# Performance work log

Measured on AMD Instinct MI355X. Metric: run time of the kernel, lower is better.

## Reference

```python
import jax, jax.numpy as jnp
import numpy as np
from jax.scipy.special import logsumexp

B, S, H, T, M = 64, 512, 768, 500, 8
POSITION_WEIGHT = 0.6
LABEL_SMOOTH = 0.1
GAMMA = 2.0


def setup_inputs() -> dict:
    key = jax.random.key(0)
    ks = jax.random.split(key, 12)
    hidden = jax.random.normal(ks[0], (B, S, H), jnp.float32)  # BERT sequence_output stand-in
    lengths = jax.random.randint(ks[1], (B,), S // 2, S + 1)
    attention_mask = (jnp.arange(S)[None, :] < lengths[:, None]).astype(jnp.int32)
    position_labels = jax.random.randint(ks[2], (B, S), 0, 3).astype(jnp.int32)
    type_labels = jax.random.randint(ks[3], (B, M), 0, T).astype(jnp.int32)
    starts = jax.random.randint(ks[4], (B, M), 1, S // 2)
    ends = starts + jax.random.randint(ks[5], (B, M), 2, 8)
    valid = jax.random.uniform(ks[6], (B, M)) < 0.8  # some (batch, span) slots unused, like the original sum()>0 filter
    target_positions = jnp.where(valid[..., None], jnp.stack([starts, ends], -1), 0).astype(jnp.int32)
    # CRF params exactly as hardcoded in __init__
    trans = jnp.array([[-5.0, 20.0, -10000.0], [-50.0, 0.0, 50.0], [0.0, -50.0, 30.0]], jnp.float32)
    start_trans = jnp.array([0.0, 0.0, -10000.0], jnp.float32)
    end_trans = jnp.array([0.0, -100.0, 0.0], jnp.float32)
    return {
        'hidden': hidden,
        'attention_mask': attention_mask,
        'position_labels': position_labels,
        'type_labels': type_labels,
        'target_positions': target_positions,
        'bi_label_weight': jnp.asarray(0.5, jnp.float32),
        'W_pos': 0.02 * jax.random.normal(ks[7], (H, 3), jnp.float32),
        'b_pos': jnp.zeros((3,), jnp.float32),
        'start_trans': start_trans,
        'end_trans': end_trans,
        'trans': trans,
        'att_W1': 0.02 * jax.random.normal(ks[8], (H, 64), jnp.float32),
        'att_b1': jnp.zeros((64,), jnp.float32),
        'att_W2': 0.02 * jax.random.normal(ks[9], (64, 1), jnp.float32),
        'att_b2': jnp.zeros((1,), jnp.float32),
        'W_type': 0.02 * jax.random.normal(ks[10], (H, T), jnp.float32),
        'b_type': jnp.zeros((T,), jnp.float32),
    }


def crf_nll(em, labels, mask, start_trans, end_trans, trans):
    # torchcrf-style masked negative log-likelihood, reduction='none'
    maskf = mask.astype(em.dtype)
    emit = jnp.take_along_axis(em, labels[..., None], -1)[..., 0]  # [B,S]
    emit_score = (emit * maskf).sum(1)
    tr = trans[labels[:, :-1], labels[:, 1:]]  # [B,S-1]
    tr_score = (tr * maskf[:, 1:]).sum(1)
    last = mask.sum(1) - 1
    last_tags = jnp.take_along_axis(labels, last[:, None], 1)[:, 0]
    score = start_trans[labels[:, 0]] + emit_score + tr_score + end_trans[last_tags]
    # log partition via scan over time
    alpha = start_trans[None, :] + em[:, 0]  # [B,3]
    def step(alpha, xs):
        em_t, m_t = xs
        nxt = logsumexp(alpha[:, :, None] + trans[None, :, :] + em_t[:, None, :], axis=1)
        return jnp.where(m_t[:, None], nxt, alpha), None
    alpha, _ = jax.lax.scan(step, alpha, (em[:, 1:].transpose(1, 0, 2), mask[:, 1:].T))
    logZ = logsumexp(alpha + end_trans[None, :], axis=-1)
    return logZ - score  # = -log_likelihood


def reference(hidden, attention_mask, position_labels, type_labels, target_positions,
              bi_label_weight, W_pos, b_pos, start_trans, end_trans, trans,
              att_W1, att_b1, att_W2, att_b2, W_type, b_type):
    mask = attention_mask.astype(bool)
    emissions = hidden @ W_pos + b_pos  # [B,S,3]
    w = jnp.where(position_labels > 0, 1.0 + bi_label_weight, 1.0)[..., None]
    em_w = emissions * w
    position_loss = crf_nll(em_w, position_labels, mask, start_trans, end_trans, trans).mean()

    # span attention pooling, batched over all (B,M) pairs instead of the Python loop
    scores = (jnp.tanh(hidden @ att_W1 + att_b1) @ att_W2 + att_b2)[..., 0]  # [B,S]
    starts = target_positions[..., 0]
    ends = target_positions[..., 1]
    valid = target_positions.sum(-1) > 0  # [B,M]
    pos = jnp.arange(hidden.shape[1])
    span_mask = (pos[None, None, :] >= starts[..., None]) & (pos[None, None, :] < ends[..., None])  # [B,M,S]
    att = jnp.where(span_mask, scores[:, None, :], -1e9)
    aw = jax.nn.softmax(att, axis=-1)  # per-span softmax == softmax over the gathered span
    pooled = jnp.einsum('bms,bsh->bmh', aw, hidden)  # [B,M,H]
    logits = pooled @ W_type + b_type  # [B,M,T]

    # label-smoothed focal loss over valid spans only
    nT = logits.shape[-1]
    onehot = jax.nn.one_hot(type_labels, nT, dtype=logits.dtype)
    smooth = onehot * (1.0 - LABEL_SMOOTH) + LABEL_SMOOTH / nT
    logp = jax.nn.log_softmax(logits, axis=-1)
    probs = jnp.exp(logp)
    ce = -(smooth * logp).sum(-1)
    pt = (smooth * probs).sum(-1)
    focal = ce * (1.0 - pt) ** GAMMA
    v = valid.astype(focal.dtype)
    type_loss = (focal * v).sum() / jnp.maximum(v.sum(), 1.0) * 10.0

    joint = POSITION_WEIGHT * position_loss + (1.0 - POSITION_WEIGHT) * type_loss
    return jnp.stack([joint, position_loss, type_loss])
```

## Files before the change

### kernel.cpp

```cpp
#include <hip/hip_runtime.h>

#define L2E 1.44269504088896340736f
#define LN2 0.69314718055994530942f
#define NEGB -1e30f

typedef float f32x4 __attribute__((ext_vector_type(4)));
typedef __bf16 bf16x8 __attribute__((ext_vector_type(8)));

static constexpr int NB = 64, NS = 512, NH = 768, NT = 500, NM = 8;

static constexpr size_t WT_ALL_OFF   = 0;
static constexpr size_t WT_TYPE_OFF  = 122880;
static constexpr size_t EM_T_OFF     = 909312;
static constexpr size_t SCORES_OFF   = 1302528;
static constexpr size_t LABELS_T_OFF = 1433600;
static constexpr size_t LEN_OFF      = 1564672;
static constexpr size_t SCAL_OFF     = 3399936;
static constexpr size_t MATM_OFF     = 3400192;
static constexpr size_t PSC_OFF      = 3547648;

__device__ __forceinline__ unsigned short f2bf(float f) {
  unsigned u = __builtin_bit_cast(unsigned, f);
  u += 0x7FFFu + ((u >> 16) & 1u);
  return (unsigned short)(u >> 16);
}
__device__ __forceinline__ float sel3(float a, float b, float c, int i) {
  return i == 0 ? a : (i == 1 ? b : c);
}
__device__ __forceinline__ float lse3(float x, float y, float z) {
  float m = fmaxf(fmaxf(x, y), z);
  float p = exp2f((x - m) * L2E) + exp2f((y - m) * L2E) + exp2f((z - m) * L2E);
  return m + log2f(p) * LN2;
}
__device__ __forceinline__ bf16x8 pack8(float4 lo, float4 hi) {
  union { unsigned u[4]; bf16x8 v; } r;
  asm("v_cvt_pk_bf16_f32 %0, %1, %2" : "=v"(r.u[0]) : "v"(lo.x), "v"(lo.y));
  asm("v_cvt_pk_bf16_f32 %0, %1, %2" : "=v"(r.u[1]) : "v"(lo.z), "v"(lo.w));
  asm("v_cvt_pk_bf16_f32 %0, %1, %2" : "=v"(r.u[2]) : "v"(hi.x), "v"(hi.y));
  asm("v_cvt_pk_bf16_f32 %0, %1, %2" : "=v"(r.u[3]) : "v"(hi.z), "v"(hi.w));
  return r.v;
}
__device__ __forceinline__ void gload_lds16(const void* g, void* l) {
  __builtin_amdgcn_global_load_lds(
      (const __attribute__((address_space(1))) unsigned*)g,
      (__attribute__((address_space(3))) unsigned*)l, 16, 0, 0);
}

__global__ __launch_bounds__(256) void ka_prep(
    const float* __restrict__ W1, const float* __restrict__ Wpos,
    const float* __restrict__ Wtype, const int* __restrict__ amask,
    unsigned short* __restrict__ wt_all, unsigned short* __restrict__ wt_type,
    int* __restrict__ lengths, float* __restrict__ scal) {
  const int bid = blockIdx.x, t = threadIdx.x;
  if (bid < 108) {
    __shared__ float tl[64][65];
    const bool is_type = bid < 96;
    const int kt = is_type ? (bid % 12) : (bid - 96);
    const int k0 = kt * 64;
    const int n0 = is_type ? (bid / 12) * 64 : 0;
    const int ld = is_type ? 500 : 64;
    const int nlim = is_type ? 500 : 64;
    const float* src = is_type ? Wtype : W1;
    unsigned short* dst = is_type ? wt_type : wt_all;
    const int n = t & 63;
    #pragma unroll
    for (int i = 0; i < 16; ++i) {
      int k = i * 4 + (t >> 6);
      tl[k][n] = (n0 + n < nlim) ? src[(size_t)(k0 + k) * ld + n0 + n] : 0.f;
    }
    __syncthreads();
    const int k = t & 63;
    #pragma unroll
    for (int i = 0; i < 16; ++i) {
      int nn = i * 4 + (t >> 6);
      dst[(size_t)(n0 + nn) * 768 + k0 + k] = f2bf(tl[k][nn]);
    }
  } else if (bid == 108) {
    for (int idx = t; idx < 16 * 768; idx += 256) {
      int n = 64 + idx / 768, k = idx % 768;
      float v = (n < 67) ? Wpos[k * 3 + (n - 64)] : 0.f;
      wt_all[(size_t)n * 768 + k] = f2bf(v);
    }
  } else {
    __shared__ int part[256];
    int bb = t >> 2, qq = t & 3;
    const int4* mp = (const int4*)(amask + bb * 512 + qq * 128);
    int s = 0;
    #pragma unroll 8
    for (int i = 0; i < 32; ++i) { int4 v = mp[i]; s += v.x + v.y + v.z + v.w; }
    part[t] = s;
    __syncthreads();
    if (qq == 0) lengths[bb] = part[t] + part[t + 1] + part[t + 2] + part[t + 3];
    if (t == 0) { scal[1] = 0.f; scal[2] = 0.f; scal[3] = 0.f; }
  }
}

__global__ __launch_bounds__(256) void k1_gemm(
    const float* __restrict__ hidden, const int* __restrict__ plab,
    const float* __restrict__ bpos, const float* __restrict__ b1,
    const float* __restrict__ W2, const float* __restrict__ b2,
    const float* __restrict__ biw, const unsigned short* __restrict__ wt_all,
    float* __restrict__ em_t, float* __restrict__ scores, int* __restrict__ labels_t) {
  __shared__ uint4 As[4][512];
  __shared__ uint4 Bs[4][512];
  const int t = threadIdx.x, w = t >> 6, l = t & 63;
  const int row0 = blockIdx.x * 64;
  const int c16 = l & 15, q = l >> 4;

  f32x4 acc[5];
  #pragma unroll
  for (int nt = 0; nt < 5; ++nt) acc[nt] = (f32x4){0.f, 0.f, 0.f, 0.f};

  auto stage = [&](int it) {
    const int bi = it & 3;
    const int k0 = it * 32;
    #pragma unroll
    for (int u = 0; u < 2; ++u) {
      int i = w * 128 + u * 64 + l;
      int row = i >> 3;
      int ss = (i & 7) ^ (row & 7);
      gload_lds16(hidden + (size_t)(row0 + row) * 768 + k0 + 4 * ss,
                  (void*)(As[bi] + (w * 128 + u * 64)));
    }
    #pragma unroll
    for (int u = 0; u < 2; ++u) {
      int i = w * 128 + u * 64 + l;
      int row = i >> 2;
      int ss = (i & 3) ^ ((row >> 1) & 3);
      gload_lds16(wt_all + (size_t)row * 768 + k0 + 8 * ss,
                  (void*)(Bs[bi] + (w * 128 + u * 64)));
    }
  };

  stage(0); stage(1);
  for (int it = 0; it < 24; ++it) {
    if (it < 22) stage(it + 2);
    if (it < 22)      asm volatile("s_waitcnt vmcnt(8)" ::: "memory");
    else if (it == 22) asm volatile("s_waitcnt vmcnt(4)" ::: "memory");
    else               asm volatile("s_waitcnt vmcnt(0)" ::: "memory");
    __builtin_amdgcn_s_barrier();
    __builtin_amdgcn_sched_barrier(0);

    const int bi = it & 3;
    const char* Ab = (const char*)As[bi];
    const char* Bb = (const char*)Bs[bi];
    const int arow = 16 * w + c16, r7 = arow & 7;
    float4 alo = *(const float4*)(Ab + arow * 128 + (((2 * q + 0) ^ r7) << 4));
    float4 ahi = *(const float4*)(Ab + arow * 128 + (((2 * q + 1) ^ r7) << 4));
    bf16x8 a = pack8(alo, ahi);
    #pragma unroll
    for (int nt = 0; nt < 5; ++nt) {
      const int brow = 16 * nt + c16;
      bf16x8 b = *(const bf16x8*)(Bb + brow * 64 + ((q ^ ((brow >> 1) & 3)) << 4));
      acc[nt] = __builtin_amdgcn_mfma_f32_16x16x32_bf16(a, b, acc[nt], 0, 0, 0);
    }
  }

  const float bias2 = b2[0];
  #pragma unroll
  for (int r = 0; r < 4; ++r) {
    float s = 0.f;
    #pragma unroll
    for (int nt = 0; nt < 4; ++nt) {
      int c = 16 * nt + c16;
      float x = acc[nt][r] + b1[c];
      float th = 1.f - 2.f / (1.f + exp2f(x * (2.f * L2E)));
      s += th * W2[c];
    }
    #pragma unroll
    for (int off = 1; off < 16; off <<= 1) s += __shfl_xor(s, off, 64);
    if (c16 == 0) {
      int row = row0 + 16 * w + 4 * q + r;
      scores[row] = s + bias2;
    }
  }
  if (c16 < 3) {
    const float bi = biw[0];
    #pragma unroll
    for (int r = 0; r < 4; ++r) {
      int row = row0 + 16 * w + 4 * q + r;
      int bb = row >> 9, ss = row & 511;
      int lab = plab[row];
      float wgt = (lab > 0) ? 1.f + bi : 1.f;
      float ev = (acc[4][r] + bpos[c16]) * wgt;
      em_t[(ss * 3 + c16) * 64 + bb] = ev;
      if (c16 == 0) labels_t[ss * 64 + bb] = lab;
    }
  }
}

__global__ __launch_bounds__(256) void kf_fused(
    const float* __restrict__ hidden, const float* __restrict__ scores,
    const int* __restrict__ tpos, const int* __restrict__ tlab,
    const unsigned short* __restrict__ wt_type, const float* __restrict__ btype,
    const float* __restrict__ em_t, const int* __restrict__ labels_t,
    const int* __restrict__ lengths, const float* __restrict__ trans,
    const float* __restrict__ strans, const float* __restrict__ etrans,
    float* __restrict__ matM, float* __restrict__ psc, float* __restrict__ scal,
    float* __restrict__ out) {
  __shared__ int last_flag;
  const int bid = blockIdx.x;
  const int t = threadIdx.x, w = t >> 6, l = t & 63;

  if (bid >= 64) {
    const int b = l, c = (bid - 64) * 4 + w;
    float T0 = trans[0], T1 = trans[1], T2 = trans[2];
    float T3 = trans[3], T4 = trans[4], T5 = trans[5];
    float T6 = trans[6], T7 = trans[7], T8 = trans[8];
    const int L = lengths[b];
    const int s0 = 8 * c;
    int labp = labels_t[(c ? (s0 - 1) : 0) * 64 + b];

    float E0[8], E1[8], E2[8]; int LB[8];
    #pragma unroll
    for (int i = 0; i < 8; ++i) {
      E0[i] = em_t[((s0 + i) * 3 + 0) * 64 + b];
      E1[i] = em_t[((s0 + i) * 3 + 1) * 64 + b];
      E2[i] = em_t[((s0 + i) * 3 + 2) * 64 + b];
      LB[i] = labels_t[(s0 + i) * 64 + b];
    }

    float M[9];
    #pragma unroll
    for (int i = 0; i < 9; ++i) M[i] = (i == 0 || i == 4 || i == 8) ? 0.f : NEGB;
    float sc = 0.f;

    #pragma unroll
    for (int i = 0; i < 8; ++i) {
      int s = s0 + i;
      bool act = (s >= 1) && (s < L);
      float N[9];
      #pragma unroll
      for (int r = 0; r < 3; ++r) {
        float ma = M[3 * r], mb = M[3 * r + 1], mc = M[3 * r + 2];
        N[3 * r + 0] = lse3(ma + T0, mb + T3, mc + T6) + E0[i];
        N[3 * r + 1] = lse3(ma + T1, mb + T4, mc + T7) + E1[i];
        N[3 * r + 2] = lse3(ma + T2, mb + T5, mc + T8) + E2[i];
      }
      #pragma unroll
      for (int r = 0; r < 9; ++r) M[r] = act ? N[r] : M[r];
      int lab = LB[i];
      float ev = sel3(E0[i], E1[i], E2[i], lab);
      float trv = sel3(sel3(T0, T1, T2, lab),
                       sel3(T3, T4, T5, lab),
                       sel3(T6, T7, T8, lab), labp);
      sc += act ? (ev + trv) : 0.f;
      labp = lab;
    }
    #pragma unroll
    for (int i = 0; i < 9; ++i) matM[(c * 9 + i) * 64 + b] = M[i];
    psc[c * 64 + b] = sc;
  } else {
    __shared__ unsigned short Apool[8][776];
    __shared__ float red[4][8][3];
    __shared__ float vl[8];
    const int b = bid;

    {
      const int sp = t >> 5;
      const int span = b * 8 + sp;
      const int st = tpos[span * 2], en = tpos[span * 2 + 1];
      const int len = (st + en > 0) ? (en - st) : 0;
      float sv[7], aw[7];
      float wm = -1e30f;
      #pragma unroll
      for (int j = 0; j < 7; ++j) {
        sv[j] = (j < len) ? scores[b * 512 + st + j] : -1e30f;
        wm = fmaxf(wm, sv[j]);
      }
      float den = 0.f;
      #pragma unroll
      for (int j = 0; j < 7; ++j) {
        aw[j] = (j < len) ? exp2f((sv[j] - wm) * L2E) : 0.f;
        den += aw[j];
      }
      float inv = (den > 0.f) ? 1.f / den : 0.f;
      #pragma unroll
      for (int j = 0; j < 7; ++j) aw[j] *= inv;

      const int h0 = (t & 31) * 24;
      float ap[24];
      #pragma unroll
      for (int i = 0; i < 24; ++i) ap[i] = 0.f;
      #pragma unroll
      for (int j = 0; j < 7; ++j) {
        if (j < len) {
          const float4* hp = (const float4*)(hidden + (size_t)(b * 512 + st + j) * 768 + h0);
          #pragma unroll
          for (int i = 0; i < 6; ++i) {
            float4 v = hp[i];
            ap[4 * i + 0] += aw[j] * v.x; ap[4 * i + 1] += aw[j] * v.y;
            ap[4 * i + 2] += aw[j] * v.z; ap[4 * i + 3] += aw[j] * v.w;
          }
        }
      }
      unsigned short* dp = &Apool[sp][h0];
      #pragma unroll
      for (int g = 0; g < 3; ++g) {
        uint4 v;
        v.x = (unsigned)f2bf(ap[8 * g + 0]) | ((unsigned)f2bf(ap[8 * g + 1]) << 16);
        v.y = (unsigned)f2bf(ap[8 * g + 2]) | ((unsigned)f2bf(ap[8 * g + 3]) << 16);
        v.z = (unsigned)f2bf(ap[8 * g + 4]) | ((unsigned)f2bf(ap[8 * g + 5]) << 16);
        v.w = (unsigned)f2bf(ap[8 * g + 6]) | ((unsigned)f2bf(ap[8 * g + 7]) << 16);
        *(uint4*)(dp + 8 * g) = v;
      }
    }
    __syncthreads();

    f32x4 acc[8];
    #pragma unroll
    for (int nt = 0; nt < 8; ++nt) acc[nt] = (f32x4){0.f, 0.f, 0.f, 0.f};
    const int arow = l & 15;
    const bf16x8 zerov = (bf16x8)(__bf16)0.f;
    for (int ks = 0; ks < 24; ++ks) {
      bf16x8 a = (arow < 8) ? *(const bf16x8*)(&Apool[arow][ks * 32 + 8 * (l >> 4)]) : zerov;
      #pragma unroll
      for (int nt = 0; nt < 8; ++nt) {
        int col = 128 * w + 16 * nt + (l & 15);
        bf16x8 bb = *(const bf16x8*)(wt_type + (size_t)col * 768 + ks * 32 + 8 * (l >> 4));
        acc[nt] = __builtin_amdgcn_mfma_f32_16x16x32_bf16(a, bb, acc[nt], 0, 0, 0);
      }
    }

    float bt[8]; bool vc[8];
    #pragma unroll
    for (int nt = 0; nt < 8; ++nt) {
      int col = 128 * w + 16 * nt + (l & 15);
      vc[nt] = col < 500;
      bt[nt] = vc[nt] ? btype[col] : 0.f;
    }
    #pragma unroll
    for (int r = 0; r < 4; ++r) {
      float lmax = -1e30f, ssum = 0.f;
      #pragma unroll
      for (int nt = 0; nt < 8; ++nt) {
        float lv = vc[nt] ? (acc[nt][r] + bt[nt]) : -1e30f;
        lmax = fmaxf(lmax, lv);
        ssum += vc[nt] ? lv : 0.f;
      }
      #pragma unroll
      for (int off = 1; off < 16; off <<= 1) lmax = fmaxf(lmax, __shfl_xor(lmax, off, 64));
      float sexp = 0.f;
      #pragma unroll
      for (int nt = 0; nt < 8; ++nt) {
        float lv = vc[nt] ? (acc[nt][r] + bt[nt]) : -1e30f;
        sexp += vc[nt] ? exp2f((lv - lmax) * L2E) : 0.f;
      }
      #pragma unroll
      for (int off = 1; off < 16; off <<= 1) {
        sexp += __shfl_xor(sexp, off, 64);
        ssum += __shfl_xor(ssum, off, 64);
      }
      if ((l & 15) == 0 && (l >> 4) < 2) {
        int row = 4 * (l >> 4) + r;
        red[w][row][0] = lmax; red[w][row][1] = sexp; red[w][row][2] = ssum;
      }
      if ((l >> 4) < 2) {
        int row = 4 * (l >> 4) + r;
        int lbl = tlab[b * 8 + row];
        if ((lbl >> 7) == w && (lbl & 15) == (l & 15)) {
          #pragma unroll
          for (int nt = 0; nt < 8; ++nt)
            if (((lbl >> 4) & 7) == nt) vl[row] = acc[nt][r] + btype[lbl];
        }
      }
    }
    __syncthreads();

    float fv = 0.f, vv = 0.f;
    if (t < 8) {
      const int row = t;
      float gm = fmaxf(fmaxf(red[0][row][0], red[1][row][0]),
                       fmaxf(red[2][row][0], red[3][row][0]));
      float sexp = 0.f, ssum = 0.f;
      #pragma unroll
      for (int i = 0; i < 4; ++i) {
        sexp += red[i][row][1] * exp2f((red[i][row][0] - gm) * L2E);
        ssum += red[i][row][2];
      }
      float logZ = gm + log2f(sexp) * LN2;
      float lp = vl[row] - logZ;
      float ce = -(0.9f * lp + 2e-4f * (ssum - 500.f * logZ));
      float pt = 0.9f * exp2f(lp * L2E) + 2e-4f;
      float focal = ce * (1.f - pt) * (1.f - pt);
      int span = b * 8 + row;
      bool valid = (tpos[span * 2] + tpos[span * 2 + 1]) > 0;
      fv = valid ? focal : 0.f;
      vv = valid ? 1.f : 0.f;
    }
    #pragma unroll
    for (int off = 1; off < 8; off <<= 1) {
      fv += __shfl_xor(fv, off, 64);
      vv += __shfl_xor(vv, off, 64);
    }
    if (t == 0) {
      atomicAdd(&scal[1], fv);
      atomicAdd(&scal[2], vv);
    }
  }

  __syncthreads();
  if (t == 0) {
    __threadfence();
    unsigned old = atomicAdd((unsigned*)&scal[3], 1u);
    last_flag = (old == 79u);
  }
  __syncthreads();
  if (last_flag && t < 64) {
    __threadfence();
    const int b = t;
    const int L = lengths[b];
    const float st0 = strans[0], st1 = strans[1], st2 = strans[2];
    const float et0 = etrans[0], et1 = etrans[1], et2 = etrans[2];
    float e00 = em_t[0 * 64 + b], e01 = em_t[1 * 64 + b], e02 = em_t[2 * 64 + b];
    int lab0 = labels_t[b];
    float a0 = st0 + e00, a1 = st1 + e01, a2 = st2 + e02;
    float score = sel3(st0, st1, st2, lab0) + sel3(e00, e01, e02, lab0);

    float cur[4][10];
    #pragma unroll
    for (int j = 0; j < 4; ++j) {
      #pragma unroll
      for (int i = 0; i < 9; ++i) cur[j][i] = matM[(j * 9 + i) * 64 + b];
      cur[j][9] = psc[j * 64 + b];
    }
    for (int r = 0; r < 16; ++r) {
      float nxt[4][10];
      if (r < 15) {
        #pragma unroll
        for (int j = 0; j < 4; ++j) {
          int c = (r + 1) * 4 + j;
          #pragma unroll
          for (int i = 0; i < 9; ++i) nxt[j][i] = matM[(c * 9 + i) * 64 + b];
          nxt[j][9] = psc[c * 64 + b];
        }
      }
      #pragma unroll
      for (int j = 0; j < 4; ++j) {
        float n0 = lse3(a0 + cur[j][0], a1 + cur[j][3], a2 + cur[j][6]);
        float n1 = lse3(a0 + cur[j][1], a1 + cur[j][4], a2 + cur[j][7]);
        float n2 = lse3(a0 + cur[j][2], a1 + cur[j][5], a2 + cur[j][8]);
        a0 = n0; a1 = n1; a2 = n2;
        score += cur[j][9];
      }
      if (r < 15) {
        #pragma unroll
        for (int j = 0; j < 4; ++j)
          #pragma unroll
          for (int i = 0; i < 10; ++i) cur[j][i] = nxt[j][i];
      }
    }
    int last = labels_t[(L - 1) * 64 + b];
    score += sel3(et0, et1, et2, last);
    float logZ = lse3(a0 + et0, a1 + et1, a2 + et2);
    float nll = logZ - score;
    #pragma unroll
    for (int off = 1; off < 64; off <<= 1) nll += __shfl_xor(nll, off, 64);
    if (b == 0) {
      float pos = nll / 64.f;
      float type = scal[1] / fmaxf(scal[2], 1.f) * 10.f;
      out[0] = 0.6f * pos + 0.4f * type;
      out[1] = pos;
      out[2] = type;
    }
  }
}

extern "C" void kernel_launch(void* const* d_in, const int* in_sizes, int n_in,
                              void* d_out, int out_size, void* d_ws, size_t ws_size,
                              hipStream_t stream) {
  const float* hidden = (const float*)d_in[0];
  const int*   amask  = (const int*)d_in[1];
  const int*   plab   = (const int*)d_in[2];
  const int*   tlab   = (const int*)d_in[3];
  const int*   tpos   = (const int*)d_in[4];
  const float* biw    = (const float*)d_in[5];
  const float* Wpos   = (const float*)d_in[6];
  const float* bpos   = (const float*)d_in[7];
  const float* strans = (const float*)d_in[8];
  const float* etrans = (const float*)d_in[9];
  const float* trans  = (const float*)d_in[10];
  const float* W1     = (const float*)d_in[11];
  const float* b1     = (const float*)d_in[12];
  const float* W2     = (const float*)d_in[13];
  const float* b2     = (const float*)d_in[14];
  const float* Wtype  = (const float*)d_in[15];
  const float* btype  = (const float*)d_in[16];
  float* out = (float*)d_out;
  char* ws = (char*)d_ws;

  unsigned short* wt_all  = (unsigned short*)(ws + WT_ALL_OFF);
  unsigned short* wt_type = (unsigned short*)(ws + WT_TYPE_OFF);
  float* em_t    = (float*)(ws + EM_T_OFF);
  float* scores  = (float*)(ws + SCORES_OFF);
  int*   labelsT = (int*)(ws + LABELS_T_OFF);
  int*   lengths = (int*)(ws + LEN_OFF);
  float* scal    = (float*)(ws + SCAL_OFF);
  float* matM    = (float*)(ws + MATM_OFF);
  float* psc     = (float*)(ws + PSC_OFF);

  ka_prep<<<110, 256, 0, stream>>>(W1, Wpos, Wtype, amask, wt_all, wt_type, lengths, scal);
  k1_gemm<<<512, 256, 0, stream>>>(hidden, plab, bpos, b1, W2, b2, biw, wt_all,
                                   em_t, scores, labelsT);
  kf_fused<<<80, 256, 0, stream>>>(hidden, scores, tpos, tlab, wt_type, btype,
                                   em_t, labelsT, lengths, trans, strans, etrans,
                                   matM, psc, scal, out);
}
```

Before: 89.04 us.

## Stage type-head weights through LDS with a multi-buffered async pipeline

The type-classification GEMM in the span blocks used to read W_type fragments straight from global memory inside the MFMA loop. It now streams 64x64 bf16 weight tiles into an 8-deep LDS ring using async global-to-LDS loads, with explicit vmcnt waits and barriers. Logits are written to shared memory, and the softmax and focal reduction is done per row across a full wavefront instead of through cross-wave partial reductions. The aim is to hide global load latency behind compute. The cost is much more LDS per block, which may limit occupancy, and a barrier at every k-step.

```diff
diff --git a/kernel.cpp b/kernel.cpp
--- a/kernel.cpp
+++ b/kernel.cpp
@@ -135,7 +135,7 @@
   stage(0); stage(1);
   for (int it = 0; it < 24; ++it) {
     if (it < 22) stage(it + 2);
-    if (it < 22)      asm volatile("s_waitcnt vmcnt(8)" ::: "memory");
+    if (it < 22)       asm volatile("s_waitcnt vmcnt(8)" ::: "memory");
     else if (it == 22) asm volatile("s_waitcnt vmcnt(4)" ::: "memory");
     else               asm volatile("s_waitcnt vmcnt(0)" ::: "memory");
     __builtin_amdgcn_s_barrier();
@@ -198,6 +198,10 @@
     const float* __restrict__ strans, const float* __restrict__ etrans,
     float* __restrict__ matM, float* __restrict__ psc, float* __restrict__ scal,
     float* __restrict__ out) {
+  __shared__ unsigned short Apool[8][776];
+  __shared__ uint4 Bt[8][512];
+  __shared__ float logitsL[8][516];
+  __shared__ float fRow[8], vRow[8];
   __shared__ int last_flag;
   const int bid = blockIdx.x;
   const int t = threadIdx.x, w = t >> 6, l = t & 63;
@@ -251,11 +255,7 @@
     for (int i = 0; i < 9; ++i) matM[(c * 9 + i) * 64 + b] = M[i];
     psc[c * 64 + b] = sc;
   } else {
-    __shared__ unsigned short Apool[8][776];
-    __shared__ float red[4][8][3];
-    __shared__ float vl[8];
     const int b = bid;
-
     {
       const int sp = t >> 5;
       const int span = b * 8 + sp;
@@ -307,93 +307,100 @@
     }
     __syncthreads();
 
-    f32x4 acc[8];
-    #pragma unroll
-    for (int nt = 0; nt < 8; ++nt) acc[nt] = (f32x4){0.f, 0.f, 0.f, 0.f};
-    const int arow = l & 15;
+    auto stageB = [&](int bi, int ct, int kt) {
+      #pragma unroll
+      for (int u = 0; u < 2; ++u) {
+        int i = u * 256 + t;
+        int row = i >> 3;
+        int ss = (i & 7) ^ (row & 7);
+        gload_lds16(wt_type + (size_t)(ct * 64 + row) * 768 + kt * 64 + 8 * ss,
+                    (void*)(Bt[bi] + i));
+      }
+    };
+    const int c16 = l & 15, q = l >> 4;
     const bf16x8 zerov = (bf16x8)(__bf16)0.f;
-    for (int ks = 0; ks < 24; ++ks) {
-      bf16x8 a = (arow < 8) ? *(const bf16x8*)(&Apool[arow][ks * 32 + 8 * (l >> 4)]) : zerov;
-      #pragma unroll
-      for (int nt = 0; nt < 8; ++nt) {
-        int col = 128 * w + 16 * nt + (l & 15);
-        bf16x8 bb = *(const bf16x8*)(wt_type + (size_t)col * 768 + ks * 32 + 8 * (l >> 4));
-        acc[nt] = __builtin_amdgcn_mfma_f32_16x16x32_bf16(a, bb, acc[nt], 0, 0, 0);
-      }
-    }
-
-    float bt[8]; bool vc[8];
-    #pragma unroll
-    for (int nt = 0; nt < 8; ++nt) {
-      int col = 128 * w + 16 * nt + (l & 15);
-      vc[nt] = col < 500;
-      bt[nt] = vc[nt] ? btype[col] : 0.f;
-    }
-    #pragma unroll
-    for (int r = 0; r < 4; ++r) {
-      float lmax = -1e30f, ssum = 0.f;
-      #pragma unroll
-      for (int nt = 0; nt < 8; ++nt) {
-        float lv = vc[nt] ? (acc[nt][r] + bt[nt]) : -1e30f;
-        lmax = fmaxf(lmax, lv);
-        ssum += vc[nt] ? lv : 0.f;
-      }
-      #pragma unroll
-      for (int off = 1; off < 16; off <<= 1) lmax = fmaxf(lmax, __shfl_xor(lmax, off, 64));
-      float sexp = 0.f;
-      #pragma unroll
-      for (int nt = 0; nt < 8; ++nt) {
-        float lv = vc[nt] ? (acc[nt][r] + bt[nt]) : -1e30f;
-        sexp += vc[nt] ? exp2f((lv - lmax) * L2E) : 0.f;
-      }
-      #pragma unroll
-      for (int off = 1; off < 16; off <<= 1) {
-        sexp += __shfl_xor(sexp, off, 64);
-        ssum += __shfl_xor(ssum, off, 64);
-      }
-      if ((l & 15) == 0 && (l >> 4) < 2) {
-        int row = 4 * (l >> 4) + r;
-        red[w][row][0] = lmax; red[w][row][1] = sexp; red[w][row][2] = ssum;
-      }
-      if ((l >> 4) < 2) {
-        int row = 4 * (l >> 4) + r;
-        int lbl = tlab[b * 8 + row];
-        if ((lbl >> 7) == w && (lbl & 15) == (l & 15)) {
-          #pragma unroll
-          for (int nt = 0; nt < 8; ++nt)
-            if (((lbl >> 4) & 7) == nt) vl[row] = acc[nt][r] + btype[lbl];
+    #pragma unroll
+    for (int s0 = 0; s0 < 6; ++s0) stageB(s0, 0, s0);
+
+    int step = 0;
+    for (int ct = 0; ct < 8; ++ct) {
+      f32x4 acc = (f32x4){0.f, 0.f, 0.f, 0.f};
+      for (int kt = 0; kt < 12; ++kt, ++step) {
+        if (step < 90) {
+          int ns = step + 6;
+          stageB(ns & 7, ns / 12, ns % 12);
+          asm volatile("s_waitcnt vmcnt(12)" ::: "memory");
         }
+        else if (step == 90) asm volatile("s_waitcnt vmcnt(10)" ::: "memory");
+        else if (step == 91) asm volatile("s_waitcnt vmcnt(8)" ::: "memory");
+        else if (step == 92) asm volatile("s_waitcnt vmcnt(6)" ::: "memory");
+        else if (step == 93) asm volatile("s_waitcnt vmcnt(4)" ::: "memory");
+        else if (step == 94) asm volatile("s_waitcnt vmcnt(2)" ::: "memory");
+        else                 asm volatile("s_waitcnt vmcnt(0)" ::: "memory");
+        __builtin_amdgcn_s_barrier();
+        __builtin_amdgcn_sched_barrier(0);
+
+        const char* Bb = (const char*)Bt[step & 7];
+        const int brow = w * 16 + c16, r7 = brow & 7;
+        bf16x8 a0 = (c16 < 8) ? *(const bf16x8*)(&Apool[c16][kt * 64 + q * 8]) : zerov;
+        bf16x8 a1 = (c16 < 8) ? *(const bf16x8*)(&Apool[c16][kt * 64 + 32 + q * 8]) : zerov;
+        bf16x8 b0 = *(const bf16x8*)(Bb + brow * 128 + (((0 + q) ^ r7) << 4));
+        bf16x8 b1 = *(const bf16x8*)(Bb + brow * 128 + (((4 + q) ^ r7) << 4));
+        acc = __builtin_amdgcn_mfma_f32_16x16x32_bf16(a0, b0, acc, 0, 0, 0);
+        acc = __builtin_amdgcn_mfma_f32_16x16x32_bf16(a1, b1, acc, 0, 0, 0);
+      }
+      if (q < 2) {
+        #pragma unroll
+        for (int r = 0; r < 4; ++r)
+          logitsL[4 * q + r][ct * 64 + w * 16 + c16] = acc[r];
       }
     }
     __syncthreads();
 
-    float fv = 0.f, vv = 0.f;
-    if (t < 8) {
-      const int row = t;
-      float gm = fmaxf(fmaxf(red[0][row][0], red[1][row][0]),
-                       fmaxf(red[2][row][0], red[3][row][0]));
-      float sexp = 0.f, ssum = 0.f;
-      #pragma unroll
-      for (int i = 0; i < 4; ++i) {
-        sexp += red[i][row][1] * exp2f((red[i][row][0] - gm) * L2E);
-        ssum += red[i][row][2];
-      }
-      float logZ = gm + log2f(sexp) * LN2;
-      float lp = vl[row] - logZ;
-      float ce = -(0.9f * lp + 2e-4f * (ssum - 500.f * logZ));
+    #pragma unroll
+    for (int rr = 0; rr < 2; ++rr) {
+      const int row = 2 * w + rr;
+      float v[8];
+      #pragma unroll
+      for (int j = 0; j < 8; ++j) {
+        int col = l + 64 * j;
+        v[j] = (col < 500) ? logitsL[row][col] + btype[col] : -1e30f;
+      }
+      float m = v[0];
+      #pragma unroll
+      for (int j = 1; j < 8; ++j) m = fmaxf(m, v[j]);
+      #pragma unroll
+      for (int off = 1; off < 64; off <<= 1) m = fmaxf(m, __shfl_xor(m, off, 64));
+      float p = 0.f, slog = 0.f;
+      #pragma unroll
+      for (int j = 0; j < 8; ++j) {
+        p += exp2f((v[j] - m) * L2E);
+        slog += (l + 64 * j < 500) ? v[j] : 0.f;
+      }
+      #pragma unroll
+      for (int off = 1; off < 64; off <<= 1) {
+        p += __shfl_xor(p, off, 64);
+        slog += __shfl_xor(slog, off, 64);
+      }
+      float logZ = m + log2f(p) * LN2;
+      int lbl = tlab[b * 8 + row];
+      float vlv = logitsL[row][lbl] + btype[lbl];
+      float lp = vlv - logZ;
+      float ce = -(0.9f * lp + 2e-4f * (slog - 500.f * logZ));
       float pt = 0.9f * exp2f(lp * L2E) + 2e-4f;
       float focal = ce * (1.f - pt) * (1.f - pt);
       int span = b * 8 + row;
       bool valid = (tpos[span * 2] + tpos[span * 2 + 1]) > 0;
-      fv = valid ? focal : 0.f;
-      vv = valid ? 1.f : 0.f;
-    }
-    #pragma unroll
-    for (int off = 1; off < 8; off <<= 1) {
-      fv += __shfl_xor(fv, off, 64);
-      vv += __shfl_xor(vv, off, 64);
-    }
+      if (l == 0) {
+        fRow[row] = valid ? focal : 0.f;
+        vRow[row] = valid ? 1.f : 0.f;
+      }
+    }
+    __syncthreads();
     if (t == 0) {
+      float fv = 0.f, vv = 0.f;
+      #pragma unroll
+      for (int i = 0; i < 8; ++i) { fv += fRow[i]; vv += vRow[i]; }
       atomicAdd(&scal[1], fv);
       atomicAdd(&scal[2], vv);
     }
```

Result: slower. 98.06 us (+10.1%).
